# Kernel tuning notes

Hardware: AMD Instinct MI355X
Metric: run time of the kernel (lower is better)

## Reference

```python
import jax, jax.numpy as jnp
import numpy as np

FEATURES = 8
MAX_LAG = 50
OMEGA, ALPHA, BETA = 0.05, 0.1, 0.85   # garch_params
NU = 4.0                               # Student-t dof (hardcoded in source)
W_ACL, W_GARCH = 10.0, 0.001           # loss_weights
LOG_2PI = float(np.log(2.0 * np.pi))


def setup_inputs() -> dict:
    key = jax.random.key(0)
    k1, k2 = jax.random.split(key)
    x_true = jax.random.normal(k1, (4096, 512, FEATURES), dtype=jnp.float32)
    dec_out = jax.random.normal(k2, (4096, 512, 2 * FEATURES), dtype=jnp.float32)
    return {"x_true": x_true, "dec_out": dec_out}


def _series(y_pred):
    # concat(seq 0 full series, last value of every other sequence) -> [T + B - 1]
    return jnp.concatenate([y_pred[0, :, 0], y_pred[1:, -1, 0]], axis=0)


def _acl_loss(y_pred):
    s = _series(y_pred)
    n = s.shape[0]
    sc = s - jnp.mean(s)
    fft_len = 2 * n
    F = jnp.fft.rfft(sc, n=fft_len)
    autocorr = jnp.fft.irfft(jnp.conj(F) * F, n=fft_len)  # real by construction
    variance = jnp.sum(jnp.square(sc))
    autocorr = autocorr[: MAX_LAG + 1] / variance
    return jnp.mean(jnp.square(autocorr[1:]))


def _garch_nll_loss(y_pred):
    s = _series(y_pred)
    r = s - jnp.mean(s)
    r2 = jnp.square(r)
    sigma0 = OMEGA / (1.0 - ALPHA - BETA)  # unconditional variance

    def step(prev_sigma_sq, cur_r2):
        new = OMEGA + ALPHA * cur_r2 + BETA * prev_sigma_sq
        return new, new

    _, cond_var = jax.lax.scan(step, sigma0, r2)
    scale = jnp.sqrt(cond_var * (NU - 2.0) / NU)
    z = r / scale
    # StudentT(df=NU, loc=0, scale).log_prob(r)
    lp = (jax.scipy.special.gammaln((NU + 1.0) / 2.0)
          - jax.scipy.special.gammaln(NU / 2.0)
          - 0.5 * jnp.log(NU * jnp.pi)
          - jnp.log(scale)
          - (NU + 1.0) / 2.0 * jnp.log1p(z * z / NU))
    return -jnp.sum(lp)


def _gaussian_nll(x_true, dec_out):
    mean = dec_out[..., :FEATURES]
    log_var = dec_out[..., FEATURES:]
    ll = -0.5 * (LOG_2PI + log_var + jnp.square(x_true - mean) * jnp.exp(-log_var))
    return -jnp.mean(jnp.sum(ll, axis=(1, 2)))


def reference(x_true, dec_out):
    y_pred = dec_out[..., :FEATURES]  # generated_x = decoder means
    recon = _gaussian_nll(x_true, dec_out)
    acl = _acl_loss(y_pred)
    garch = _garch_nll_loss(y_pred)
    return recon + W_ACL * acl + W_GARCH * garch
```

## Files before the change

### kernel.cpp

```cpp
#include <hip/hip_runtime.h>

#define NS        4607
#define NRECON    8192
#define NTAIL     51
#define N_TOTAL   16777216.0

#define WS_PART   0
#define WS_GARCH  8192
#define WS_ACL    8193

__device__ __forceinline__ float wave_sum(float v) {
    for (int o = 32; o > 0; o >>= 1) v += __shfl_down(v, o);
    return v;
}

__global__ __launch_bounds__(256) void main_kernel(
    const float* __restrict__ x, const float* __restrict__ dec,
    float* __restrict__ ws)
{
    const int tid  = threadIdx.x;
    const int lane = tid & 63;
    const int wv   = tid >> 6;

    if (blockIdx.x >= NTAIL) {
        const int tile = blockIdx.x - NTAIL;
        const long long pixBase = (long long)tile * 256;
        const float4* dec4 = (const float4*)(dec + pixBase * 16);
        const float4* x4   = (const float4*)(x + pixBase * 8);

        float4 dv[4], xv[4];
#pragma unroll
        for (int r = 0; r < 4; ++r) {
            const int w = tid + r * 256;
            dv[r] = dec4[w];
            const int u = ((w >> 2) << 1) | (w & 1);
            xv[r] = x4[u];
        }

        float acc = 0.f;
#pragma unroll
        for (int r = 0; r < 4; ++r) {
            const int w = tid + r * 256;
            const int q = w & 3;
            float4 a = dv[r], b;
            b.x = __shfl_xor(a.x, 2);
            b.y = __shfl_xor(a.y, 2);
            b.z = __shfl_xor(a.z, 2);
            b.w = __shfl_xor(a.w, 2);
            const bool im = (q < 2);
            float4 m, lv;
            m.x  = im ? a.x : b.x;  m.y  = im ? a.y : b.y;
            m.z  = im ? a.z : b.z;  m.w  = im ? a.w : b.w;
            lv.x = im ? b.x : a.x;  lv.y = im ? b.y : a.y;
            lv.z = im ? b.z : a.z;  lv.w = im ? b.w : a.w;
            float4 xx = xv[r];
            float d;
            d = xx.x - m.x; acc += lv.x + d * d * __expf(-lv.x);
            d = xx.y - m.y; acc += lv.y + d * d * __expf(-lv.y);
            d = xx.z - m.z; acc += lv.z + d * d * __expf(-lv.z);
            d = xx.w - m.w; acc += lv.w + d * d * __expf(-lv.w);
        }

        acc = wave_sum(acc);
        __shared__ float p4[4];
        if (lane == 0) p4[wv] = acc;
        __syncthreads();
        if (tid == 0) ws[WS_PART + tile] = 0.5f * (p4[0] + p4[1] + p4[2] + p4[3]);
    } else {
        const float OMEGA = 0.05f, ALPHA = 0.1f, BETA = 0.85f;
        __shared__ float sc[NS];
        __shared__ float s4[4];

        float lsum = 0.f;
        for (int j = tid; j < NS; j += 256) {
            float v = (j < 512) ? dec[(long long)j * 16]
                                : dec[(long long)(j - 511) * 8192 + 8176];
            sc[j] = v;
            lsum += v;
        }
        lsum = wave_sum(lsum);
        __syncthreads();
        if (lane == 0) s4[wv] = lsum;
        __syncthreads();
        const float mean = (s4[0] + s4[1] + s4[2] + s4[3]) / (float)NS;

        float vsum = 0.f;
        __syncthreads();
        for (int j = tid; j < NS; j += 256) { float v = sc[j] - mean; sc[j] = v; vsum += v * v; }
        vsum = wave_sum(vsum);
        __syncthreads();
        if (lane == 0) s4[wv] = vsum;
        __syncthreads();
        const float var = s4[0] + s4[1] + s4[2] + s4[3];

        if (blockIdx.x == 0) {
            const int start = tid * 18;
            const int end   = min(start + 18, NS);
            float e = 0.f, p = 1.f;
            for (int i = start; i < end; ++i) {
                float r2 = sc[i] * sc[i];
                e = (OMEGA + ALPHA * r2) + BETA * e;
                p *= BETA;
            }
            for (int o = 1; o < 64; o <<= 1) {
                float pe = __shfl_up(e, o), pp = __shfl_up(p, o);
                if (lane >= o) { e = e + p * pe; p = p * pp; }
            }
            __shared__ float wE[4], wP[4];
            if (lane == 63) { wE[wv] = e; wP[wv] = p; }
            __syncthreads();
            float cE = 0.f, cP = 1.f;
            for (int t = 0; t < wv; ++t) { cE = wE[t] + wP[t] * cE; cP = wP[t] * cP; }
            float eE = __shfl_up(e, 1), eP = __shfl_up(p, 1);
            if (lane == 0) { eE = 0.f; eP = 1.f; }
            float prev = (eE + eP * cE) + (eP * cP) * 1.0f;
            float g = 0.f;
            for (int i = start; i < end; ++i) {
                float r2 = sc[i] * sc[i];
                float cv = OMEGA + ALPHA * r2 + BETA * prev;
                prev = cv;
                g += 0.5f * logf(0.5f * cv) + 2.5f * log1pf(r2 / (2.f * cv));
            }
            g = wave_sum(g);
            __syncthreads();
            if (lane == 0) s4[wv] = g;
            __syncthreads();
            if (tid == 0) ws[WS_GARCH] = s4[0] + s4[1] + s4[2] + s4[3];
        } else {
            const int k = blockIdx.x;
            float a = 0.f;
            for (int i = tid; i < NS - k; i += 256) a += sc[i] * sc[i + k];
            a = wave_sum(a);
            __syncthreads();
            if (lane == 0) s4[wv] = a;
            __syncthreads();
            if (tid == 0) {
                float r = (s4[0] + s4[1] + s4[2] + s4[3]) / var;
                ws[WS_ACL + (k - 1)] = r * r;
            }
        }
    }
}

__global__ __launch_bounds__(256) void final_kernel(
    const float* __restrict__ ws, float* __restrict__ out)
{
    const int tid  = threadIdx.x;
    const int lane = tid & 63;
    const int wv   = tid >> 6;
    __shared__ double d4[4];
    __shared__ float  aclbuf[1];

    double ds = 0.0;
    for (int i = tid; i < NRECON; i += 256) ds += (double)ws[WS_PART + i];
    for (int o = 32; o > 0; o >>= 1) ds += __shfl_down(ds, o);
    if (lane == 0) d4[wv] = ds;

    if (wv == 0) {
        float av = (lane < 50) ? ws[WS_ACL + lane] : 0.f;
        av = wave_sum(av);
        if (lane == 0) aclbuf[0] = av;
    }
    __syncthreads();

    if (tid == 0) {
        const double LOG_2PI = 1.8378770664093453;
        const double NEG_C   = 0.9808292530117262;
        double q = d4[0] + d4[1] + d4[2] + d4[3];
        double recon = 0.5 * (q + N_TOTAL * LOG_2PI) / 4096.0;
        double acl   = (double)aclbuf[0] / 50.0;
        double garch = (double)ws[WS_GARCH] + (double)NS * NEG_C;
        out[0] = (float)(recon + 10.0 * acl + 0.001 * garch);
    }
}

extern "C" void kernel_launch(void* const* d_in, const int* in_sizes, int n_in,
                              void* d_out, int out_size, void* d_ws, size_t ws_size,
                              hipStream_t stream) {
    const float* x_true  = (const float*)d_in[0];
    const float* dec_out = (const float*)d_in[1];
    float* ws  = (float*)d_ws;
    float* out = (float*)d_out;

    main_kernel<<<NRECON + NTAIL, 256, 0, stream>>>(x_true, dec_out, ws);
    final_kernel<<<1, 256, 0, stream>>>(ws, out);
}
```

Before: 246.1 us.

## Move ACF scratch to global memory, coarsen recon blocks, drop duplicate exp work

The 18 KB LDS array for the centered series, which had been reserved by every block including the recon tiles, becomes a per-block slice of global workspace so recon blocks no longer pay LDS-limited occupancy. Each recon block now processes four 256-pixel tiles, which cuts the grid from 8192 to 2048 recon blocks. Inputs are read with nontemporal loads. The per-element math is rewritten so each lane handles only its own two features, removing the duplicated exp and FMA work and the 0.5 rescale. The trade-off is that the tail blocks now do their series scratch work through global memory, and the workspace must hold the extra scratch region.

```diff
diff --git a/kernel.cpp b/kernel.cpp
--- a/kernel.cpp
+++ b/kernel.cpp
@@ -1,13 +1,18 @@
 #include <hip/hip_runtime.h>
 
 #define NS        4607
-#define NRECON    8192
 #define NTAIL     51
+#define RBLK      2048
+#define TPB       4
 #define N_TOTAL   16777216.0
 
 #define WS_PART   0
-#define WS_GARCH  8192
-#define WS_ACL    8193
+#define WS_GARCH  RBLK
+#define WS_ACL    (RBLK + 1)
+#define WS_SCR    (RBLK + 64)
+#define SCR_STRIDE 4672
+
+typedef float vf4 __attribute__((ext_vector_type(4)));
 
 __device__ __forceinline__ float wave_sum(float v) {
     for (int o = 32; o > 0; o >>= 1) v += __shfl_down(v, o);
@@ -21,61 +26,63 @@
     const int tid  = threadIdx.x;
     const int lane = tid & 63;
     const int wv   = tid >> 6;
+    __shared__ float s4[4];
 
     if (blockIdx.x >= NTAIL) {
-        const int tile = blockIdx.x - NTAIL;
-        const long long pixBase = (long long)tile * 256;
-        const float4* dec4 = (const float4*)(dec + pixBase * 16);
-        const float4* x4   = (const float4*)(x + pixBase * 8);
+        const int rb = blockIdx.x - NTAIL;
+        float acc = 0.f;
 
-        float4 dv[4], xv[4];
+        for (int t = 0; t < TPB; ++t) {
+            const long long pixBase = ((long long)(rb * TPB + t)) * 256;
+            const vf4* dp = (const vf4*)(dec + pixBase * 16);
+            const vf4* xp = (const vf4*)(x + pixBase * 8);
+
+            vf4 dv[4], xv[4];
 #pragma unroll
-        for (int r = 0; r < 4; ++r) {
-            const int w = tid + r * 256;
-            dv[r] = dec4[w];
-            const int u = ((w >> 2) << 1) | (w & 1);
-            xv[r] = x4[u];
-        }
+            for (int r = 0; r < 4; ++r) {
+                const int w = tid + r * 256;
+                dv[r] = __builtin_nontemporal_load(dp + w);
+                xv[r] = __builtin_nontemporal_load(xp + (((w >> 2) << 1) | (w & 1)));
+            }
+            asm volatile("" ::: "memory");
 
-        float acc = 0.f;
 #pragma unroll
-        for (int r = 0; r < 4; ++r) {
-            const int w = tid + r * 256;
-            const int q = w & 3;
-            float4 a = dv[r], b;
-            b.x = __shfl_xor(a.x, 2);
-            b.y = __shfl_xor(a.y, 2);
-            b.z = __shfl_xor(a.z, 2);
-            b.w = __shfl_xor(a.w, 2);
-            const bool im = (q < 2);
-            float4 m, lv;
-            m.x  = im ? a.x : b.x;  m.y  = im ? a.y : b.y;
-            m.z  = im ? a.z : b.z;  m.w  = im ? a.w : b.w;
-            lv.x = im ? b.x : a.x;  lv.y = im ? b.y : a.y;
-            lv.z = im ? b.z : a.z;  lv.w = im ? b.w : a.w;
-            float4 xx = xv[r];
-            float d;
-            d = xx.x - m.x; acc += lv.x + d * d * __expf(-lv.x);
-            d = xx.y - m.y; acc += lv.y + d * d * __expf(-lv.y);
-            d = xx.z - m.z; acc += lv.z + d * d * __expf(-lv.z);
-            d = xx.w - m.w; acc += lv.w + d * d * __expf(-lv.w);
+            for (int r = 0; r < 4; ++r) {
+                const int w = tid + r * 256;
+                const int q = w & 3;
+                vf4 a = dv[r], b;
+                b.x = __shfl_xor(a.x, 2);
+                b.y = __shfl_xor(a.y, 2);
+                b.z = __shfl_xor(a.z, 2);
+                b.w = __shfl_xor(a.w, 2);
+                const bool im = (q < 2);
+                vf4 xx = xv[r];
+                float xe0 = im ? xx.x : xx.z;
+                float me0 = im ? a.x  : b.z;
+                float le0 = im ? b.x  : a.z;
+                float xe1 = im ? xx.y : xx.w;
+                float me1 = im ? a.y  : b.w;
+                float le1 = im ? b.y  : a.w;
+                float d0 = xe0 - me0;
+                float d1 = xe1 - me1;
+                acc += le0 + d0 * d0 * __expf(-le0);
+                acc += le1 + d1 * d1 * __expf(-le1);
+            }
         }
 
         acc = wave_sum(acc);
-        __shared__ float p4[4];
-        if (lane == 0) p4[wv] = acc;
+        if (lane == 0) s4[wv] = acc;
         __syncthreads();
-        if (tid == 0) ws[WS_PART + tile] = 0.5f * (p4[0] + p4[1] + p4[2] + p4[3]);
+        if (tid == 0) ws[WS_PART + rb] = s4[0] + s4[1] + s4[2] + s4[3];
     } else {
         const float OMEGA = 0.05f, ALPHA = 0.1f, BETA = 0.85f;
-        __shared__ float sc[NS];
-        __shared__ float s4[4];
+        float* scr = ws + WS_SCR + blockIdx.x * SCR_STRIDE;
 
         float lsum = 0.f;
         for (int j = tid; j < NS; j += 256) {
             float v = (j < 512) ? dec[(long long)j * 16]
                                 : dec[(long long)(j - 511) * 8192 + 8176];
-            sc[j] = v;
+            scr[j] = v;
             lsum += v;
         }
         lsum = wave_sum(lsum);
@@ -86,7 +93,11 @@
 
         float vsum = 0.f;
         __syncthreads();
-        for (int j = tid; j < NS; j += 256) { float v = sc[j] - mean; sc[j] = v; vsum += v * v; }
+        for (int j = tid; j < NS; j += 256) {
+            float v = scr[j] - mean;
+            scr[j] = v;
+            vsum += v * v;
+        }
         vsum = wave_sum(vsum);
         __syncthreads();
         if (lane == 0) s4[wv] = vsum;
@@ -98,7 +109,7 @@
             const int end   = min(start + 18, NS);
             float e = 0.f, p = 1.f;
             for (int i = start; i < end; ++i) {
-                float r2 = sc[i] * sc[i];
+                float r2 = scr[i] * scr[i];
                 e = (OMEGA + ALPHA * r2) + BETA * e;
                 p *= BETA;
             }
@@ -116,7 +127,7 @@
             float prev = (eE + eP * cE) + (eP * cP) * 1.0f;
             float g = 0.f;
             for (int i = start; i < end; ++i) {
-                float r2 = sc[i] * sc[i];
+                float r2 = scr[i] * scr[i];
                 float cv = OMEGA + ALPHA * r2 + BETA * prev;
                 prev = cv;
                 g += 0.5f * logf(0.5f * cv) + 2.5f * log1pf(r2 / (2.f * cv));
@@ -129,7 +140,7 @@
         } else {
             const int k = blockIdx.x;
             float a = 0.f;
-            for (int i = tid; i < NS - k; i += 256) a += sc[i] * sc[i + k];
+            for (int i = tid; i < NS - k; i += 256) a += scr[i] * scr[i + k];
             a = wave_sum(a);
             __syncthreads();
             if (lane == 0) s4[wv] = a;
@@ -152,7 +163,7 @@
     __shared__ float  aclbuf[1];
 
     double ds = 0.0;
-    for (int i = tid; i < NRECON; i += 256) ds += (double)ws[WS_PART + i];
+    for (int i = tid; i < RBLK; i += 256) ds += (double)ws[WS_PART + i];
     for (int o = 32; o > 0; o >>= 1) ds += __shfl_down(ds, o);
     if (lane == 0) d4[wv] = ds;
 
@@ -182,6 +193,6 @@
     float* ws  = (float*)d_ws;
     float* out = (float*)d_out;
 
-    main_kernel<<<NRECON + NTAIL, 256, 0, stream>>>(x_true, dec_out, ws);
+    main_kernel<<<RBLK + NTAIL, 256, 0, stream>>>(x_true, dec_out, ws);
     final_kernel<<<1, 256, 0, stream>>>(ws, out);
 }
```

After: 229.9 us. -6.6%, faster.
